# Kernel tuning notes

Measured on AMD Instinct MI355X. Metric: run time of the kernel, lower is better.

## Reference

```python
import jax, jax.numpy as jnp
import numpy as np

N, E, D, EF, C, G, NPG = 50000, 500000, 16, 8, 10, 500, 100
NUM_LAYERS = 3
EPS = 1e-5


def setup_inputs() -> dict:
    key = jax.random.key(0)
    ks = jax.random.split(key, 16)
    s = 0.1
    return {
        'x': jax.random.normal(ks[0], (N, D), jnp.float32),
        'edge_attr': jax.random.normal(ks[1], (E, EF), jnp.float32),
        # edge MLP (shared across all NNConv layers, as in the source)
        'edge_w1': jax.random.normal(ks[2], (EF, D), jnp.float32) * s,
        'edge_b1': jnp.zeros((D,), jnp.float32),
        'edge_w2': jax.random.normal(ks[3], (D, D * D), jnp.float32) * s,
        'edge_b2': jnp.zeros((D * D,), jnp.float32),
        # per-layer NNConv root weight + bias
        'root': jax.random.normal(ks[4], (NUM_LAYERS, D, D), jnp.float32) * s,
        'conv_bias': jnp.zeros((NUM_LAYERS, D), jnp.float32),
        # per-layer BatchNorm affine params
        'bn_gamma': jnp.ones((NUM_LAYERS, D), jnp.float32),
        'bn_beta': jnp.zeros((NUM_LAYERS, D), jnp.float32),
        # readout MLP
        'fc1_w': jax.random.normal(ks[5], (4 * D, D), jnp.float32) * s,
        'fc1_b': jnp.zeros((D,), jnp.float32),
        'fc2_w': jax.random.normal(ks[6], (D, C), jnp.float32) * s,
        'fc2_b': jnp.zeros((C,), jnp.float32),
        # graph structure (constants w.r.t. grads)
        'edge_index': jax.random.randint(ks[7], (2, E), 0, N, dtype=jnp.int32),
        'lengths': jnp.full((G,), NPG, dtype=jnp.int32),
    }


def reference(x, edge_attr, edge_w1, edge_b1, edge_w2, edge_b2, root,
              conv_bias, bn_gamma, bn_beta, fc1_w, fc1_b, fc2_w, fc2_b,
              edge_index, lengths):
    src, dst = edge_index[0], edge_index[1]
    # Edge MLP -> per-edge weight matrices [E, D, D] (edge_attr is layer-invariant,
    # so the shared edge_model output is computed once).
    h_e = jnp.tanh(edge_attr @ edge_w1 + edge_b1)
    W = (h_e @ edge_w2 + edge_b2).reshape(E, D, D)
    # in-degree for mean aggregation (nodes with no incoming edges -> 0)
    deg = jax.ops.segment_sum(jnp.ones((E,), x.dtype), dst, num_segments=N)
    deg = jnp.maximum(deg, 1.0)[:, None]

    h = x
    for l in range(NUM_LAYERS):
        # NNConv: gather -> per-edge matvec -> scatter-mean, plus root term + bias
        msg = jnp.einsum('ei,eio->eo', h[src], W)          # [E, D]
        agg = jax.ops.segment_sum(msg, dst, num_segments=N) / deg
        h = agg + h @ root[l] + conv_bias[l]
        # BatchNorm over nodes (training-mode batch statistics, biased var)
        mu = h.mean(axis=0)
        var = h.var(axis=0)
        h = (h - mu) * jax.lax.rsqrt(var + EPS) * bn_gamma[l] + bn_beta[l]
        h = jnp.tanh(h)  # Dropout is identity in eval mode

    hidden = h
    # ragged segment pooling: graph id per node from lengths
    seg = jnp.repeat(jnp.arange(G), lengths, total_repeat_length=N)
    sum_p = jax.ops.segment_sum(hidden, seg, num_segments=G)
    cnt = jnp.maximum(lengths.astype(hidden.dtype), 1)[:, None]
    mean_p = sum_p / cnt
    max_p = jax.ops.segment_max(hidden, seg, num_segments=G)
    min_p = jax.ops.segment_min(hidden, seg, num_segments=G)
    pooled = jnp.concatenate([mean_p, max_p, min_p, sum_p], axis=1)  # [G, 4D]

    fc = jnp.tanh(pooled @ fc1_w + fc1_b)
    fc = fc @ fc2_w + fc2_b
    out = jax.nn.log_softmax(fc, axis=1)
    return hidden, pooled, fc, out
```

## Files before the change

### kernel.cpp

```cpp
#include <hip/hip_runtime.h>

#define D 16
#define EFD 8
#define NREP 64
#define TSTRIDE 272

typedef unsigned short u16;
typedef unsigned int u32;

__device__ __forceinline__ u16 f2bf(float x) {
    u32 u = __float_as_uint(x);
    u += 0x7fffu + ((u >> 16) & 1u);
    return (u16)(u >> 16);
}
__device__ __forceinline__ void unpack8(uint4 u, float* f) {
    f[0] = __uint_as_float(u.x << 16); f[1] = __uint_as_float(u.x & 0xffff0000u);
    f[2] = __uint_as_float(u.y << 16); f[3] = __uint_as_float(u.y & 0xffff0000u);
    f[4] = __uint_as_float(u.z << 16); f[5] = __uint_as_float(u.z & 0xffff0000u);
    f[6] = __uint_as_float(u.w << 16); f[7] = __uint_as_float(u.w & 0xffff0000u);
}


__global__ void k_zero2(int* a, int na, float* b, int nb) {
    int i = blockIdx.x * 256 + threadIdx.x;
    if (i < na) a[i] = 0;
    if (i < nb) b[i] = 0.f;
}


__global__ void k_rank2(const int* __restrict__ src, const int* __restrict__ dst,
                        int* __restrict__ cntS, int* __restrict__ cntD,
                        int* __restrict__ rankS, int* __restrict__ rankD, int E_) {
    int e = blockIdx.x * 256 + threadIdx.x;
    if (e < E_) {
        rankS[e] = atomicAdd(&cntS[src[e]], 1);
        rankD[e] = atomicAdd(&cntD[dst[e]], 1);
    }
}


__global__ void k_scanA2(const int* __restrict__ cnt2, int* __restrict__ offs2,
                         int* __restrict__ bsum2, int n, int nScan) {
    __shared__ int s[1024];
    int half = blockIdx.x / nScan;
    int blk  = blockIdx.x % nScan;
    const int* c = cnt2 + (size_t)half * n;
    int* of = offs2 + (size_t)half * (n + 1);
    int* bs = bsum2 + half * 64;
    int i = blk * 1024 + threadIdx.x;
    int v = (i < n) ? c[i] : 0;
    s[threadIdx.x] = v;
    __syncthreads();
    for (int d = 1; d < 1024; d <<= 1) {
        int t = (threadIdx.x >= d) ? s[threadIdx.x - d] : 0;
        __syncthreads();
        s[threadIdx.x] += t;
        __syncthreads();
    }
    int incl = s[threadIdx.x];
    if (i < n) of[i] = incl - v;
    if (threadIdx.x == 1023) bs[blk] = incl;
}

__global__ void k_scanC2(int* __restrict__ offs2, const int* __restrict__ bsum2,
                         int n, int nScan, int total) {
    __shared__ int s[64];
    int half = blockIdx.x / nScan;
    int blk  = blockIdx.x % nScan;
    int* of = offs2 + (size_t)half * (n + 1);
    const int* bs = bsum2 + half * 64;
    if (threadIdx.x < 64) s[threadIdx.x] = (threadIdx.x < nScan) ? bs[threadIdx.x] : 0;
    __syncthreads();
    if (threadIdx.x < 64) {
        for (int d = 1; d < 64; d <<= 1) {
            int t = (threadIdx.x >= d) ? s[threadIdx.x - d] : 0;
            __syncthreads();
            s[threadIdx.x] += t;
            __syncthreads();
        }
    } else {
        for (int d = 1; d < 64; d <<= 1) { __syncthreads(); __syncthreads(); }
    }
    int base = (blk == 0) ? 0 : s[blk - 1];
    int i = blk * 1024 + threadIdx.x;
    if (i < n) of[i] += base;
    else if (i == n) of[n] = total;
}


__global__ void k_place_he(const int* __restrict__ src, const int* __restrict__ dst,
                           const int* __restrict__ rankS, const int* __restrict__ rankD,
                           const int* __restrict__ offsS, const int* __restrict__ offsD,
                           const float* __restrict__ ea, const float* __restrict__ w1,
                           const float* __restrict__ b1,
                           u16* __restrict__ hE, int* __restrict__ permInv, int E_) {
    __shared__ float w1s[EFD * D];
    __shared__ float b1s[D];
    if (threadIdx.x < EFD * D) w1s[threadIdx.x] = w1[threadIdx.x];
    if (threadIdx.x < D) b1s[threadIdx.x] = b1[threadIdx.x];
    __syncthreads();
    int e = blockIdx.x * 256 + threadIdx.x;
    if (e >= E_) return;
    int p = offsS[src[e]] + rankS[e];
    int q = offsD[dst[e]] + rankD[e];
    permInv[p] = q;
    const float4* a4 = (const float4*)(ea + (size_t)e * EFD);
    float4 x0 = a4[0], x1 = a4[1];
    u32 pk[8];
#pragma unroll
    for (int v = 0; v < 8; v++) {
        float o0, o1;
#pragma unroll
        for (int h = 0; h < 2; h++) {
            int o = 2 * v + h;
            float u0 = x0.x * w1s[0 * D + o] + x0.y * w1s[1 * D + o]
                     + x0.z * w1s[2 * D + o] + x0.w * w1s[3 * D + o];
            float u1 = x1.x * w1s[4 * D + o] + x1.y * w1s[5 * D + o]
                     + x1.z * w1s[6 * D + o] + x1.w * w1s[7 * D + o];
            float t = tanhf(b1s[o] + u0 + u1);
            if (h == 0) o0 = t; else o1 = t;
        }
        pk[v] = (u32)f2bf(o0) | ((u32)f2bf(o1) << 16);
    }
    uint4* h8 = (uint4*)(hE + (size_t)p * D);
    h8[0] = make_uint4(pk[0], pk[1], pk[2], pk[3]);
    h8[1] = make_uint4(pk[4], pk[5], pk[6], pk[7]);
}


#define SBSTRIDE 17

__global__ void k_Tmsg(const float* __restrict__ hin, const float* __restrict__ statsPrev,
                       const float* __restrict__ gamma, const float* __restrict__ beta,
                       float* __restrict__ hout, const float* __restrict__ w2,
                       const float* __restrict__ b2, const u16* __restrict__ hE,
                       const int* __restrict__ offsS, const int* __restrict__ permInv,
                       u16* __restrict__ msg, int n, int useBN) {
    __shared__ float hs[16 * D];
    __shared__ float Tt[16 * TSTRIDE];
    __shared__ float sstats[32];
    __shared__ uint4 sbuf[4 * 2 * 4 * SBSTRIDE + 4];
    int tid = threadIdx.x;
    int j = tid >> 4, o = tid & 15;
    int w = tid >> 6, jj = j & 3;
    int base = blockIdx.x * 16;
    int node = base + j;
    float fn = (float)n;
    int p0 = 0, p1 = 0;
    if (node < n) { p0 = offsS[node]; p1 = offsS[node + 1]; }
    int deg = p1 - p0;
    int nCh = (deg + 7) >> 3;
    uint4* buf0 = &sbuf[((w * 2 + 0) * 4 + jj) * SBSTRIDE];
    uint4* buf1 = &sbuf[((w * 2 + 1) * 4 + jj) * SBSTRIDE];

    uint4 regH = make_uint4(0, 0, 0, 0);
    int regQ = 0;
    if (deg > 0) {
        int pr = p0 + (o >> 1);
        int pc = (pr < p1) ? pr : p1 - 1;
        regH = ((const uint4*)(hE + (size_t)pc * D))[o & 1];
        if (o < 8) {
            int pq = p0 + o;
            regQ = permInv[(pq < p1) ? pq : p1 - 1];
        }
    }

    float w16[16], b16[16];
#pragma unroll
    for (int i = 0; i < 16; i++) w16[i] = w2[j * 256 + i * 16 + o];
#pragma unroll
    for (int i = 0; i < 16; i++) b16[i] = b2[i * 16 + o];
    if (useBN && tid < 32) {
        float a = 0.f;
#pragma unroll 8
        for (int r = 0; r < NREP; r++) a += statsPrev[r * 32 + tid];
        sstats[tid] = a;
    }
    __syncthreads();
    {
        float hv = 0.f;
        if (node < n) {
            float xin = hin[(size_t)node * D + o];
            if (useBN) {
                float mu = sstats[o] / fn;
                float var = sstats[16 + o] / fn - mu * mu;
                hv = tanhf((xin - mu) * rsqrtf(var + 1e-5f) * gamma[o] + beta[o]);
                hout[(size_t)node * D + o] = hv;
            } else {
                hv = xin;
            }
        }
        hs[tid] = hv;
    }
    __syncthreads();
    {
        const float4* hs4 = (const float4*)hs;
#pragma unroll
        for (int nb = 0; nb < 16; nb++) {
            float4 h0 = hs4[nb * 4 + 0], h1 = hs4[nb * 4 + 1];
            float4 h2 = hs4[nb * 4 + 2], h3 = hs4[nb * 4 + 3];
            float q0 = h0.x * w16[0]  + h0.y * w16[1]  + h0.z * w16[2]  + h0.w * w16[3];
            float q1 = h1.x * w16[4]  + h1.y * w16[5]  + h1.z * w16[6]  + h1.w * w16[7];
            float q2 = h2.x * w16[8]  + h2.y * w16[9]  + h2.z * w16[10] + h2.w * w16[11];
            float q3 = h3.x * w16[12] + h3.y * w16[13] + h3.z * w16[14] + h3.w * w16[15];
            Tt[nb * TSTRIDE + tid] = (q0 + q1) + (q2 + q3);
        }
        float4 h0 = hs4[j * 4 + 0], h1 = hs4[j * 4 + 1];
        float4 h2 = hs4[j * 4 + 2], h3 = hs4[j * 4 + 3];
        float q0 = h0.x * b16[0]  + h0.y * b16[1]  + h0.z * b16[2]  + h0.w * b16[3];
        float q1 = h1.x * b16[4]  + h1.y * b16[5]  + h1.z * b16[6]  + h1.w * b16[7];
        float q2 = h2.x * b16[8]  + h2.y * b16[9]  + h2.z * b16[10] + h2.w * b16[11];
        float q3 = h3.x * b16[12] + h3.y * b16[13] + h3.z * b16[14] + h3.w * b16[15];
        Tt[j * TSTRIDE + 256 + o] = (q0 + q1) + (q2 + q3);
    }
    __syncthreads();
    if (node < n && deg > 0) {
        float tr[16];
#pragma unroll
        for (int j2 = 0; j2 < 16; j2++) tr[j2] = Tt[j * TSTRIDE + j2 * 16 + o];
        float tb = Tt[j * TSTRIDE + 256 + o];
        buf0[o] = regH;
        for (int c = 0; c < nCh; c++) {
            uint4* cur = (c & 1) ? buf1 : buf0;
            uint4* nxt = (c & 1) ? buf0 : buf1;
            uint4 nH; int nQ = 0;
            if (c + 1 < nCh) {
                int pr = p0 + (c + 1) * 8 + (o >> 1);
                int pc = (pr < p1) ? pr : p1 - 1;
                nH = ((const uint4*)(hE + (size_t)pc * D))[o & 1];
                if (o < 8) {
                    int pq = p0 + (c + 1) * 8 + o;
                    nQ = permInv[(pq < p1) ? pq : p1 - 1];
                }
            }
            int eMax = deg - c * 8;
            if (eMax > 8) eMax = 8;
            for (int i = 0; i < eMax; i++) {
                uint4 r0 = cur[2 * i], r1 = cur[2 * i + 1];
                int qe = __shfl(regQ, jj * 16 + i);
                float e[16];
                unpack8(r0, e); unpack8(r1, e + 8);
                float s0 = e[0]  * tr[0]  + e[1]  * tr[1]  + e[2]  * tr[2]  + e[3]  * tr[3];
                float s1 = e[4]  * tr[4]  + e[5]  * tr[5]  + e[6]  * tr[6]  + e[7]  * tr[7];
                float s2 = e[8]  * tr[8]  + e[9]  * tr[9]  + e[10] * tr[10] + e[11] * tr[11];
                float s3 = e[12] * tr[12] + e[13] * tr[13] + e[14] * tr[14] + e[15] * tr[15];
                msg[(size_t)qe * D + o] = f2bf(tb + ((s0 + s1) + (s2 + s3)));
            }
            if (c + 1 < nCh) {
                nxt[o] = nH;
                regQ = nQ;
            }
        }
    }
}


__global__ void k_agg(const float* __restrict__ h, const u16* __restrict__ msg,
                      const int* __restrict__ offsD, const float* __restrict__ root_l,
                      const float* __restrict__ cbias, float* __restrict__ hpre,
                      float* __restrict__ statsR, int n) {
    __shared__ float rootS[D * D];
    __shared__ float red[256], red2[256];
    if (threadIdx.x < D * D) rootS[threadIdx.x] = root_l[threadIdx.x];
    __syncthreads();
    int slot = threadIdx.x >> 4, o = threadIdx.x & 15;
    int node = blockIdx.x * 16 + slot;
    float acc = 0.f;
    if (node < n) {
        int p0 = offsD[node], p1 = offsD[node + 1];
        float sum = 0.f;
        int p = p0;
        for (; p + 8 <= p1; p += 8) {
            float a0 = __uint_as_float((u32)msg[(size_t)(p + 0) * D + o] << 16);
            float a1 = __uint_as_float((u32)msg[(size_t)(p + 1) * D + o] << 16);
            float a2 = __uint_as_float((u32)msg[(size_t)(p + 2) * D + o] << 16);
            float a3 = __uint_as_float((u32)msg[(size_t)(p + 3) * D + o] << 16);
            float a4 = __uint_as_float((u32)msg[(size_t)(p + 4) * D + o] << 16);
            float a5 = __uint_as_float((u32)msg[(size_t)(p + 5) * D + o] << 16);
            float a6 = __uint_as_float((u32)msg[(size_t)(p + 6) * D + o] << 16);
            float a7 = __uint_as_float((u32)msg[(size_t)(p + 7) * D + o] << 16);
            sum += ((a0 + a1) + (a2 + a3)) + ((a4 + a5) + (a6 + a7));
        }
        for (; p < p1; p++) sum += __uint_as_float((u32)msg[(size_t)p * D + o] << 16);
        float deg = (float)((p1 - p0) > 1 ? (p1 - p0) : 1);
        const float* hr = h + (size_t)node * D;
        float r0 = hr[0]  * rootS[0 * D + o]  + hr[1]  * rootS[1 * D + o]
                 + hr[2]  * rootS[2 * D + o]  + hr[3]  * rootS[3 * D + o];
        float r1 = hr[4]  * rootS[4 * D + o]  + hr[5]  * rootS[5 * D + o]
                 + hr[6]  * rootS[6 * D + o]  + hr[7]  * rootS[7 * D + o];
        float r2 = hr[8]  * rootS[8 * D + o]  + hr[9]  * rootS[9 * D + o]
                 + hr[10] * rootS[10 * D + o] + hr[11] * rootS[11 * D + o];
        float r3 = hr[12] * rootS[12 * D + o] + hr[13] * rootS[13 * D + o]
                 + hr[14] * rootS[14 * D + o] + hr[15] * rootS[15 * D + o];
        acc = sum / deg + cbias[o] + ((r0 + r1) + (r2 + r3));
        hpre[(size_t)node * D + o] = acc;
    }
    red[threadIdx.x] = acc;
    red2[threadIdx.x] = acc * acc;
    __syncthreads();
    for (int off = 128; off >= 16; off >>= 1) {
        if (threadIdx.x < off) {
            red[threadIdx.x] += red[threadIdx.x + off];
            red2[threadIdx.x] += red2[threadIdx.x + off];
        }
        __syncthreads();
    }
    if (threadIdx.x < 32) {
        float v = (threadIdx.x < 16) ? red[threadIdx.x] : red2[threadIdx.x - 16];
        atomicAdd(&statsR[(blockIdx.x & (NREP - 1)) * 32 + threadIdx.x], v);
    }
}


__global__ void k_readout(const float* __restrict__ hpre, const float* __restrict__ statsR,
                          const float* __restrict__ gamma, const float* __restrict__ beta,
                          const int* __restrict__ lengths,
                          const float* __restrict__ w1, const float* __restrict__ b1,
                          const float* __restrict__ w2, const float* __restrict__ b2,
                          float* __restrict__ outHidden, float* __restrict__ outPooled,
                          float* __restrict__ fcOut, float* __restrict__ lsmOut,
                          int Gc, int n) {
    __shared__ int sl[512];
    __shared__ float sstats[32];
    int tid = threadIdx.x;
    int g = blockIdx.x;
    if (tid < 32) {
        float a = 0.f;
#pragma unroll 8
        for (int r = 0; r < NREP; r++) a += statsR[r * 32 + tid];
        sstats[tid] = a;
    }
    int v = (tid < Gc) ? lengths[tid] : 0;
    sl[tid] = v;
    __syncthreads();
    for (int d = 1; d < 512; d <<= 1) {
        int t = (tid >= d) ? sl[tid - d] : 0;
        __syncthreads();
        sl[tid] += t;
        __syncthreads();
    }
    int n1 = sl[g];
    int n0 = n1 - lengths[g];
    float fn = (float)n;
    int slot = tid >> 4, o = tid & 15;
    float mu = sstats[o] / fn;
    float var = sstats[16 + o] / fn - mu * mu;
    float rstd = rsqrtf(var + 1e-5f);
    float gm = gamma[o], bt = beta[o];
    float s = 0.f, mx = -3.402823466e38f, mn = 3.402823466e38f;
    for (int nd = n0 + slot; nd < n1; nd += 32) {
        float xin = hpre[(size_t)nd * D + o];
        float x = tanhf((xin - mu) * rstd * gm + bt);
        outHidden[(size_t)nd * D + o] = x;
        s += x;
        mx = fmaxf(mx, x);
        mn = fminf(mn, x);
    }
    __shared__ float rs[512], rmx[512], rmn[512];
    rs[tid] = s; rmx[tid] = mx; rmn[tid] = mn;
    __syncthreads();
    for (int off = 256; off >= 16; off >>= 1) {
        if (tid < off) {
            rs[tid] += rs[tid + off];
            rmx[tid] = fmaxf(rmx[tid], rmx[tid + off]);
            rmn[tid] = fminf(rmn[tid], rmn[tid + off]);
        }
        __syncthreads();
    }
    __shared__ float p64[64], t16[16], f10[10];
    __shared__ float mred, lred;
    if (tid < 16) {
        float cnt = fmaxf((float)(n1 - n0), 1.f);
        float sum = rs[tid];
        float* row = outPooled + (size_t)g * 64;
        float mean = sum / cnt;
        p64[tid] = mean;          row[tid] = mean;
        p64[16 + tid] = rmx[tid]; row[16 + tid] = rmx[tid];
        p64[32 + tid] = rmn[tid]; row[32 + tid] = rmn[tid];
        p64[48 + tid] = sum;      row[48 + tid] = sum;
    }
    __syncthreads();
    if (tid < 16) {
        float a = b1[tid];
        for (int k = 0; k < 64; k++) a += p64[k] * w1[k * 16 + tid];
        t16[tid] = tanhf(a);
    }
    __syncthreads();
    if (tid < 10) {
        float a = b2[tid];
        for (int oo = 0; oo < 16; oo++) a += t16[oo] * w2[oo * 10 + tid];
        f10[tid] = a;
        fcOut[(size_t)g * 10 + tid] = a;
    }
    __syncthreads();
    if (tid == 0) {
        float m = f10[0];
        for (int c = 1; c < 10; c++) m = fmaxf(m, f10[c]);
        float se = 0.f;
        for (int c = 0; c < 10; c++) se += expf(f10[c] - m);
        mred = m;
        lred = logf(se);
    }
    __syncthreads();
    if (tid < 10)
        lsmOut[(size_t)g * 10 + tid] = f10[tid] - mred - lred;
}


extern "C" void kernel_launch(void* const* d_in, const int* in_sizes, int n_in,
                              void* d_out, int out_size, void* d_ws, size_t ws_size,
                              hipStream_t stream) {
    const float* x    = (const float*)d_in[0];
    const float* ea   = (const float*)d_in[1];
    const float* ew1  = (const float*)d_in[2];
    const float* eb1  = (const float*)d_in[3];
    const float* ew2  = (const float*)d_in[4];
    const float* eb2  = (const float*)d_in[5];
    const float* root = (const float*)d_in[6];
    const float* cb   = (const float*)d_in[7];
    const float* gam  = (const float*)d_in[8];
    const float* bet  = (const float*)d_in[9];
    const float* f1w  = (const float*)d_in[10];
    const float* f1b  = (const float*)d_in[11];
    const float* f2w  = (const float*)d_in[12];
    const float* f2b  = (const float*)d_in[13];
    const int* eidx   = (const int*)d_in[14];
    const int* lens   = (const int*)d_in[15];

    int N  = in_sizes[0] / D;
    int E_ = in_sizes[1] / EFD;
    int Gc = in_sizes[15];
    const int* srcIdx = eidx;
    const int* dstIdx = eidx + E_;

    float* outHidden = (float*)d_out;
    float* outPooled = outHidden + (size_t)N * D;
    float* outFc     = outPooled + (size_t)Gc * 4 * D;
    float* outLsm    = outFc + (size_t)Gc * 10;

    char* wsp = (char*)d_ws;
    size_t off = 0;
    auto alloc = [&](size_t bytes) -> void* {
        void* p = wsp + off;
        off = (off + bytes + 255) & ~(size_t)255;
        return p;
    };
    int*   cnt2    = (int*)alloc((size_t)2 * N * 4);
    int*   offs2   = (int*)alloc((size_t)2 * (N + 1) * 4);
    int*   bsum2   = (int*)alloc(128 * 4);
    int*   rankS   = (int*)alloc((size_t)E_ * 4);
    int*   rankD   = (int*)alloc((size_t)E_ * 4);
    int*   permInv = (int*)alloc((size_t)E_ * 4);
    u16*   hE      = (u16*)alloc((size_t)E_ * D * 2);
    u16*   msg     = (u16*)alloc((size_t)E_ * D * 2);
    float* bufA    = (float*)alloc((size_t)N * D * 4);
    float* tmp     = (float*)alloc((size_t)N * D * 4);
    float* statsR3 = (float*)alloc((size_t)3 * NREP * 32 * 4);

    int* offsS = offs2;
    int* offsD = offs2 + (N + 1);
    int nScan = (N + 1023) / 1024;

    k_zero2<<<(2 * N + 255) / 256, 256, 0, stream>>>(cnt2, 2 * N, statsR3, 3 * NREP * 32);
    k_rank2<<<(E_ + 255) / 256, 256, 0, stream>>>(srcIdx, dstIdx, cnt2, cnt2 + N,
                                                  rankS, rankD, E_);
    k_scanA2<<<2 * nScan, 1024, 0, stream>>>(cnt2, offs2, bsum2, N, nScan);
    k_scanC2<<<2 * nScan, 1024, 0, stream>>>(offs2, bsum2, N, nScan, E_);
    k_place_he<<<(E_ + 255) / 256, 256, 0, stream>>>(srcIdx, dstIdx, rankS, rankD,
                                                     offsS, offsD, ea, ew1, eb1,
                                                     hE, permInv, E_);

    for (int l = 0; l < 3; l++) {
        const float* hin   = (l == 0) ? x : tmp;
        const float* hroot = (l == 0) ? x : bufA;
        float* statsCur = statsR3 + (size_t)l * NREP * 32;
        const float* statsPrev = statsR3 + (size_t)(l - 1) * NREP * 32;
        k_Tmsg<<<(N + 15) / 16, 256, 0, stream>>>(
            hin, (l == 0) ? nullptr : statsPrev,
            (l == 0) ? nullptr : gam + (size_t)(l - 1) * 16,
            (l == 0) ? nullptr : bet + (size_t)(l - 1) * 16,
            bufA, ew2, eb2, hE, offsS, permInv, msg, N, (l == 0) ? 0 : 1);
        k_agg<<<(N + 15) / 16, 256, 0, stream>>>(hroot, msg, offsD,
                                                 root + (size_t)l * 256, cb + (size_t)l * 16,
                                                 tmp, statsCur, N);
    }

    k_readout<<<Gc, 512, 0, stream>>>(tmp, statsR3 + (size_t)2 * NREP * 32,
                                      gam + 32, bet + 32, lens, f1w, f1b, f2w, f2b,
                                      outHidden, outPooled, outFc, outLsm, Gc, N);
}
```

Baseline: 287.2 us.

## Compute per-node transform table with bf16 MFMA instead of scalar FMAs

Replaces the per-thread scalar dot products that build the per-node T table (h times edge_w2 and b2) with a 16x16x32 bf16 MFMA. Each block first converts w2 and b2 into a bf16 B-fragment layout in shared memory, and the 16 node rows are packed as the A fragment. The result tiles are written into Tt, whose stride is changed to limit bank conflicts. This reduces the FP32 ALU work in that stage, but every block now re-converts the full weight table and h and the weights are rounded to bf16, which costs precision.

```diff
diff --git a/kernel.cpp b/kernel.cpp
--- a/kernel.cpp
+++ b/kernel.cpp
@@ -3,10 +3,12 @@
 #define D 16
 #define EFD 8
 #define NREP 64
-#define TSTRIDE 272
+#define TSTRIDE 276
 
 typedef unsigned short u16;
 typedef unsigned int u32;
+typedef __attribute__((ext_vector_type(8))) short short8;
+typedef __attribute__((ext_vector_type(4))) float f32x4;
 
 __device__ __forceinline__ u16 f2bf(float x) {
     u32 u = __float_as_uint(x);
@@ -139,10 +141,12 @@
     __shared__ float hs[16 * D];
     __shared__ float Tt[16 * TSTRIDE];
     __shared__ float sstats[32];
+    __shared__ u16 Bls[17 * 32 * 8];
     __shared__ uint4 sbuf[4 * 2 * 4 * SBSTRIDE + 4];
     int tid = threadIdx.x;
     int j = tid >> 4, o = tid & 15;
     int w = tid >> 6, jj = j & 3;
+    int lane = tid & 63;
     int base = blockIdx.x * 16;
     int node = base + j;
     float fn = (float)n;
@@ -165,11 +169,15 @@
         }
     }
 
-    float w16[16], b16[16];
-#pragma unroll
-    for (int i = 0; i < 16; i++) w16[i] = w2[j * 256 + i * 16 + o];
-#pragma unroll
-    for (int i = 0; i < 16; i++) b16[i] = b2[i * 16 + o];
+    for (int e = tid; e < 17 * 256; e += 256) {
+        int t = e >> 8, rem = e & 255;
+        int l = rem >> 3, jb = rem & 7;
+        int k = ((l >> 4) << 3) + jb;
+        int c = (t << 4) + (l & 15);
+        float v = (c < 256) ? w2[((c >> 4) << 8) + (k << 4) + (c & 15)]
+                            : b2[(k << 4) + (c - 256)];
+        Bls[e] = f2bf(v);
+    }
     if (useBN && tid < 32) {
         float a = 0.f;
 #pragma unroll 8
@@ -194,24 +202,24 @@
     }
     __syncthreads();
     {
-        const float4* hs4 = (const float4*)hs;
+        int quad = lane >> 4;
+        int m = lane & 15;
+        short8 afr = {0, 0, 0, 0, 0, 0, 0, 0};
+        if (quad < 2) {
+            const float* hp = &hs[m * 16 + quad * 8];
 #pragma unroll
-        for (int nb = 0; nb < 16; nb++) {
-            float4 h0 = hs4[nb * 4 + 0], h1 = hs4[nb * 4 + 1];
-            float4 h2 = hs4[nb * 4 + 2], h3 = hs4[nb * 4 + 3];
-            float q0 = h0.x * w16[0]  + h0.y * w16[1]  + h0.z * w16[2]  + h0.w * w16[3];
-            float q1 = h1.x * w16[4]  + h1.y * w16[5]  + h1.z * w16[6]  + h1.w * w16[7];
-            float q2 = h2.x * w16[8]  + h2.y * w16[9]  + h2.z * w16[10] + h2.w * w16[11];
-            float q3 = h3.x * w16[12] + h3.y * w16[13] + h3.z * w16[14] + h3.w * w16[15];
-            Tt[nb * TSTRIDE + tid] = (q0 + q1) + (q2 + q3);
-        }
-        float4 h0 = hs4[j * 4 + 0], h1 = hs4[j * 4 + 1];
-        float4 h2 = hs4[j * 4 + 2], h3 = hs4[j * 4 + 3];
-        float q0 = h0.x * b16[0]  + h0.y * b16[1]  + h0.z * b16[2]  + h0.w * b16[3];
-        float q1 = h1.x * b16[4]  + h1.y * b16[5]  + h1.z * b16[6]  + h1.w * b16[7];
-        float q2 = h2.x * b16[8]  + h2.y * b16[9]  + h2.z * b16[10] + h2.w * b16[11];
-        float q3 = h3.x * b16[12] + h3.y * b16[13] + h3.z * b16[14] + h3.w * b16[15];
-        Tt[j * TSTRIDE + 256 + o] = (q0 + q1) + (q2 + q3);
+            for (int i = 0; i < 8; i++) afr[i] = (short)f2bf(hp[i]);
+        }
+        for (int t = w; t < 17; t += 4) {
+            short8 bfr = {0, 0, 0, 0, 0, 0, 0, 0};
+            if (quad < 2) bfr = *(const short8*)&Bls[(t * 32 + lane) * 8];
+            f32x4 cfr = {0.f, 0.f, 0.f, 0.f};
+            cfr = __builtin_amdgcn_mfma_f32_16x16x32_bf16(afr, bfr, cfr, 0, 0, 0);
+            int cbase = t * 16 + m;
+#pragma unroll
+            for (int r = 0; r < 4; r++)
+                Tt[(quad * 4 + r) * TSTRIDE + cbase] = cfr[r];
+        }
     }
     __syncthreads();
     if (node < n && deg > 0) {
```

Result: slower. 317.7 us (+10.6%).
